# Kernel optimization log

Measured on AMD Instinct MI355X. Metric: run time of the kernel, lower is better.

Reference implementation:

```python
import jax, jax.numpy as jnp
import numpy as np

K = 3
C = 256
C4 = C // 4


def adaptive_avg_pool(x, k):
    # Faithful torch AdaptiveAvgPool2d: bin i covers [floor(i*H/k), ceil((i+1)*H/k))
    N, Ch, H, W = x.shape
    rows = []
    for i in range(k):
        sh, eh = (i * H) // k, -((-(i + 1) * H) // k)
        cols = []
        for j in range(k):
            sw, ew = (j * W) // k, -((-(j + 1) * W) // k)
            cols.append(x[:, :, sh:eh, sw:ew].mean(axis=(2, 3)))
        rows.append(jnp.stack(cols, axis=-1))  # [N,Ch,k]
    return jnp.stack(rows, axis=-2)  # [N,Ch,k,k]


def setup_inputs() -> dict:
    key = jax.random.key(0)
    ks = jax.random.split(key, 6)
    x = jax.random.normal(ks[0], (16, C, 128, 128), dtype=jnp.float32)
    # 1x1 convs stored as dense matrices (spatial 1x1 squeezed)
    conv_w = jax.random.normal(ks[1], (C4, C), dtype=jnp.float32) * (1.0 / np.sqrt(C))
    conv_b = jax.random.normal(ks[2], (C4,), dtype=jnp.float32) * 0.02
    dw_b = jax.random.normal(ks[3], (C4,), dtype=jnp.float32) * 0.02
    fuse_w = jax.random.normal(ks[4], (C, C4), dtype=jnp.float32) * (1.0 / np.sqrt(C4))
    fuse_b = jax.random.normal(ks[5], (C,), dtype=jnp.float32) * 0.02
    return {"x": x, "conv_w": conv_w, "conv_b": conv_b, "dw_b": dw_b,
            "fuse_w": fuse_w, "fuse_b": fuse_b}


def reference(x, conv_w, conv_b, dw_b, fuse_w, fuse_b):
    N, Ch, H, W = x.shape
    k = K
    c4 = conv_w.shape[0]
    # f = conv(x)  (1x1)
    f = jnp.einsum('nchw,oc->nohw', x, conv_w) + conv_b[None, :, None, None]
    # g = conv(pool(x)) -> per-sample depthwise filters [N, C4, k, k]
    xp = adaptive_avg_pool(x, k)
    g = jnp.einsum('nchw,oc->nohw', xp, conv_w) + conv_b[None, :, None, None]
    # batched dynamic depthwise conv: fold batch into groups, one fused conv
    p = (k - 1) // 2
    lhs = f.reshape(1, N * c4, H, W)
    rhs = g.reshape(N * c4, 1, k, k)
    y = jax.lax.conv_general_dilated(
        lhs, rhs, window_strides=(1, 1), padding=[(p, p), (p, p)],
        feature_group_count=N * c4,
        dimension_numbers=('NCHW', 'OIHW', 'NCHW'))
    y = y.reshape(N, c4, H, W) + dw_b[None, :, None, None]
    # fuse (1x1)
    out = jnp.einsum('nchw,oc->nohw', y, fuse_w) + fuse_b[None, :, None, None]
    return out
```

## Files before the change

kernel.cpp:

```cpp
#include <hip/hip_runtime.h>
#include <hip/hip_bf16.h>

#define NB 16
#define C 256
#define C4 64
#define HDIM 128
#define WDIM 128
#define HW 16384

typedef __bf16 bf16x8 __attribute__((ext_vector_type(8)));
typedef float f32x4 __attribute__((ext_vector_type(4)));

__device__ __forceinline__ unsigned short f2bf(float x) {
    union { __bf16 h; unsigned short u; } c;
    c.h = (__bf16)x;
    return c.u;
}
__device__ __forceinline__ float bf2f(unsigned short b) {
    union { float f; unsigned u; } a; a.u = ((unsigned)b) << 16; return a.f;
}

__global__ __launch_bounds__(256) void k0_pack(
    const float* __restrict__ conv_w, const float* __restrict__ fuse_w,
    const float* __restrict__ fuse_b, const float* __restrict__ dw_b,
    unsigned short* __restrict__ cwpk, unsigned short* __restrict__ fwpk,
    float* __restrict__ fbe)
{
    int tid = blockIdx.x * 256 + threadIdx.x;
    {
        int m = tid >> 8, k = tid & 255;
        int frag = (m >> 4) * 8 + (k >> 5);
        int lane = (m & 15) | (((k >> 3) & 3) << 4);
        int e = k & 7;
        cwpk[(frag * 64 + lane) * 8 + e] = f2bf(conv_w[m * 256 + k]);
    }
    {
        int m = tid >> 6, k = tid & 63;
        int frag = (m >> 4) * 2 + (k >> 5);
        int lane = (m & 15) | (((k >> 3) & 3) << 4);
        int e = k & 7;
        fwpk[(frag * 64 + lane) * 8 + e] = f2bf(fuse_w[m * 64 + k]);
    }
    if (tid < 256) {
        float s = fuse_b[tid];
        #pragma unroll
        for (int o = 0; o < 64; ++o) s += fuse_w[tid * 64 + o] * dw_b[o];
        fbe[tid] = s;
    }
}

__global__ __launch_bounds__(256) void k1_conv(
    const float* __restrict__ x, const unsigned short* __restrict__ cwpk,
    const float* __restrict__ conv_b, unsigned short* __restrict__ f_ws)
{
    __shared__ unsigned short xlds[32 * 138];
    int blk = blockIdx.x;
    int n = blk >> 7;
    int p0 = (blk & 127) * WDIM;
    int t = threadIdx.x;
    int lane = t & 63, wv = t >> 6, gq = lane >> 4, l15 = lane & 15;
    const float* xn = x + (size_t)n * C * HW + p0;

    int lch = t >> 5;
    int lpx = (t & 31) * 4;

    f32x4 r[4];
    #pragma unroll
    for (int j = 0; j < 4; ++j)
        r[j] = __builtin_nontemporal_load(
            reinterpret_cast<const f32x4*>(&xn[(size_t)(j * 8 + lch) * HW + lpx]));

    f32x4 acc[2][4];
    #pragma unroll
    for (int pt = 0; pt < 2; ++pt)
        #pragma unroll
        for (int m = 0; m < 4; ++m) acc[pt][m] = (f32x4){0.f, 0.f, 0.f, 0.f};

    for (int kc = 0; kc < 8; ++kc) {
        unsigned int pk[4][2];
        #pragma unroll
        for (int j = 0; j < 4; ++j) {
            pk[j][0] = ((unsigned)f2bf(r[j].y) << 16) | f2bf(r[j].x);
            pk[j][1] = ((unsigned)f2bf(r[j].w) << 16) | f2bf(r[j].z);
        }
        __syncthreads();
        #pragma unroll
        for (int j = 0; j < 4; ++j) {
            unsigned int* dst = reinterpret_cast<unsigned int*>(
                &xlds[(j * 8 + lch) * 138 + lpx]);
            dst[0] = pk[j][0];
            dst[1] = pk[j][1];
        }
        __syncthreads();
        if (kc < 7) {
            #pragma unroll
            for (int j = 0; j < 4; ++j)
                r[j] = __builtin_nontemporal_load(
                    reinterpret_cast<const f32x4*>(
                        &xn[(size_t)((kc + 1) * 32 + j * 8 + lch) * HW + lpx]));
        }
        bf16x8 a[4];
        #pragma unroll
        for (int m = 0; m < 4; ++m)
            a[m] = *reinterpret_cast<const bf16x8*>(cwpk + ((m * 8 + kc) * 64 + lane) * 8);
        #pragma unroll
        for (int pt = 0; pt < 2; ++pt) {
            int px = wv * 32 + pt * 16 + l15;
            union { bf16x8 v; unsigned short u[8]; } b;
            #pragma unroll
            for (int e = 0; e < 8; ++e)
                b.u[e] = xlds[(gq * 8 + e) * 138 + px];
            #pragma unroll
            for (int m = 0; m < 4; ++m)
                acc[pt][m] = __builtin_amdgcn_mfma_f32_16x16x32_bf16(a[m], b.v, acc[pt][m], 0, 0, 0);
        }
    }

    unsigned short* fn = f_ws + (size_t)n * C4 * HW;
    #pragma unroll
    for (int pt = 0; pt < 2; ++pt) {
        int px = p0 + wv * 32 + pt * 16 + l15;
        #pragma unroll
        for (int m = 0; m < 4; ++m) {
            #pragma unroll
            for (int e = 0; e < 4; ++e) {
                int o = m * 16 + gq * 4 + e;
                fn[(size_t)o * HW + px] = f2bf(acc[pt][m][e] + conv_b[o]);
            }
        }
    }
}

__global__ __launch_bounds__(256) void k2_pool(
    const unsigned short* __restrict__ f_ws, float* __restrict__ g_ws)
{
    int no = blockIdx.x;
    const unsigned short* fp = f_ws + (size_t)no * HW;
    int tid = threadIdx.x;
    float s[9];
    #pragma unroll
    for (int k = 0; k < 9; ++k) s[k] = 0.f;

    for (int it = 0; it < 8; ++it) {
        int p = (it * 256 + tid) * 8;
        int h = p >> 7, wbase = p & 127;
        union { uint4 q; unsigned short u[8]; } d;
        d.q = *reinterpret_cast<const uint4*>(fp + p);
        float cs0 = 0.f, cs1 = 0.f, cs2 = 0.f;
        #pragma unroll
        for (int z = 0; z < 8; ++z) {
            float v = bf2f(d.u[z]);
            int w = wbase + z;
            if (w < 43)            cs0 += v;
            if (w >= 42 && w < 86) cs1 += v;
            if (w >= 85)           cs2 += v;
        }
        if (h < 43)            { s[0] += cs0; s[1] += cs1; s[2] += cs2; }
        if (h >= 42 && h < 86) { s[3] += cs0; s[4] += cs1; s[5] += cs2; }
        if (h >= 85)           { s[6] += cs0; s[7] += cs1; s[8] += cs2; }
    }

    __shared__ float red[4][9];
    int lane = tid & 63, wv = tid >> 6;
    #pragma unroll
    for (int k = 0; k < 9; ++k) {
        float v = s[k];
        for (int off = 32; off > 0; off >>= 1) v += __shfl_down(v, off, 64);
        s[k] = v;
    }
    if (lane == 0) {
        #pragma unroll
        for (int k = 0; k < 9; ++k) red[wv][k] = s[k];
    }
    __syncthreads();
    if (tid < 9) {
        const int cnt[3] = {43, 44, 43};
        float tot = red[0][tid] + red[1][tid] + red[2][tid] + red[3][tid];
        int i = tid / 3, j = tid - 3 * i;
        g_ws[no * 9 + tid] = tot / (float)(cnt[i] * cnt[j]);
    }
}

__global__ __launch_bounds__(512) void k3_dwfuse(
    const unsigned short* __restrict__ f_ws, const float* __restrict__ g_ws,
    const unsigned short* __restrict__ fwpk, const float* __restrict__ fbe,
    float* __restrict__ out)
{
    __shared__ unsigned short ylds[64][136];
    int blk = blockIdx.x;
    int n = blk >> 7;
    int h = blk & 127;
    int t = threadIdx.x;

    {
        int o = t >> 3, q = t & 7;
        int wb = q * 16;
        const unsigned short* fp = f_ws + (size_t)(n * 64 + o) * HW;
        const float* gp = g_ws + (n * 64 + o) * 9;
        float gv[9];
        #pragma unroll
        for (int k = 0; k < 9; ++k) gv[k] = gp[k];
        float y[16];
        #pragma unroll
        for (int i = 0; i < 16; ++i) y[i] = 0.f;
        #pragma unroll
        for (int dy = -1; dy <= 1; ++dy) {
            int hh = h + dy;
            if (hh < 0 || hh >= HDIM) continue;
            const unsigned short* row = fp + hh * WDIM;
            union { uint4 q4; unsigned short u[8]; } bA, bB;
            bA.q4 = *reinterpret_cast<const uint4*>(row + wb);
            bB.q4 = *reinterpret_cast<const uint4*>(row + wb + 8);
            float lft = bf2f(row[wb == 0 ? 0 : wb - 1]);
            if (wb == 0)   lft = 0.f;
            float rgt = bf2f(row[wb == 112 ? 127 : wb + 16]);
            if (wb == 112) rgt = 0.f;
            float rv[18];
            rv[0] = lft;
            #pragma unroll
            for (int z = 0; z < 8; ++z) rv[1 + z] = bf2f(bA.u[z]);
            #pragma unroll
            for (int z = 0; z < 8; ++z) rv[9 + z] = bf2f(bB.u[z]);
            rv[17] = rgt;
            float g0 = gv[(dy + 1) * 3], g1 = gv[(dy + 1) * 3 + 1], g2 = gv[(dy + 1) * 3 + 2];
            #pragma unroll
            for (int i = 0; i < 16; ++i)
                y[i] += g0 * rv[i] + g1 * rv[i + 1] + g2 * rv[i + 2];
        }
        union { uint4 q4[2]; unsigned short u[16]; } pk;
        #pragma unroll
        for (int i = 0; i < 16; ++i) pk.u[i] = f2bf(y[i]);
        *reinterpret_cast<uint4*>(&ylds[o][wb])     = pk.q4[0];
        *reinterpret_cast<uint4*>(&ylds[o][wb + 8]) = pk.q4[1];
    }
    __syncthreads();

    int lane = t & 63, wv = t >> 6, gq = lane >> 4;
    int chb = (wv & 3) * 64, pxb = (wv >> 2) * 64;
    f32x4 acc[4][4];
    #pragma unroll
    for (int a = 0; a < 4; ++a)
        #pragma unroll
        for (int b = 0; b < 4; ++b) acc[a][b] = (f32x4){0.f,0.f,0.f,0.f};

    #pragma unroll
    for (int kc = 0; kc < 2; ++kc) {
        bf16x8 bfr[4];
        #pragma unroll
        for (int pj = 0; pj < 4; ++pj) {
            union { bf16x8 v; unsigned short u[8]; } bb;
            #pragma unroll
            for (int e = 0; e < 8; ++e)
                bb.u[e] = ylds[kc * 32 + gq * 8 + e][pxb + pj * 16 + (lane & 15)];
            bfr[pj] = bb.v;
        }
        #pragma unroll
        for (int mc = 0; mc < 4; ++mc) {
            int mtile = (wv & 3) * 4 + mc;
            bf16x8 a = *reinterpret_cast<const bf16x8*>(
                fwpk + ((mtile * 2 + kc) * 64 + lane) * 8);
            #pragma unroll
            for (int pj = 0; pj < 4; ++pj)
                acc[mc][pj] = __builtin_amdgcn_mfma_f32_16x16x32_bf16(a, bfr[pj], acc[mc][pj], 0, 0, 0);
        }
    }

    size_t outbase = (size_t)n * C * HW + (size_t)h * WDIM;
    #pragma unroll
    for (int mc = 0; mc < 4; ++mc) {
        #pragma unroll
        for (int e = 0; e < 4; ++e) {
            int c = chb + mc * 16 + gq * 4 + e;
            float bias = fbe[c];
            #pragma unroll
            for (int pj = 0; pj < 4; ++pj) {
                int w = pxb + pj * 16 + (lane & 15);
                out[outbase + (size_t)c * HW + w] = acc[mc][pj][e] + bias;
            }
        }
    }
}

extern "C" void kernel_launch(void* const* d_in, const int* in_sizes, int n_in,
                              void* d_out, int out_size, void* d_ws, size_t ws_size,
                              hipStream_t stream) {
    const float* x      = (const float*)d_in[0];
    const float* conv_w = (const float*)d_in[1];
    const float* conv_b = (const float*)d_in[2];
    const float* dw_b   = (const float*)d_in[3];
    const float* fuse_w = (const float*)d_in[4];
    const float* fuse_b = (const float*)d_in[5];
    float* out = (float*)d_out;

    char* ws = (char*)d_ws;
    unsigned short* f_ws = (unsigned short*)ws;
    float* g_ws          = (float*)(ws + 33554432);
    unsigned short* cwpk = (unsigned short*)(ws + 33554432 + 36864);
    unsigned short* fwpk = (unsigned short*)(ws + 33554432 + 36864 + 32768);
    float* fbe           = (float*)(ws + 33554432 + 36864 + 32768 + 32768);

    k0_pack<<<dim3(64), dim3(256), 0, stream>>>(conv_w, fuse_w, fuse_b, dw_b, cwpk, fwpk, fbe);
    k1_conv<<<dim3(2048), dim3(256), 0, stream>>>(x, cwpk, conv_b, f_ws);
    k2_pool<<<dim3(1024), dim3(256), 0, stream>>>(f_ws, g_ws);
    k3_dwfuse<<<dim3(2048), dim3(512), 0, stream>>>(f_ws, g_ws, fwpk, fbe, out);
}
```

Measured before the change: 140.8 us.

## Fuse adaptive pooling into conv kernel via atomics and vectorize stores

Removes the separate pooling kernel by accumulating per-row bin sums inside the 1x1 conv kernel and adding them into a zeroed global buffer with atomics; the depthwise kernel then scales by the bin counts. MFMA operands are swapped so each lane holds contiguous pixels, which allows packed 8-byte bf16 stores of f and 16-byte float4 stores of the output. This saves a full re-read of the f workspace and one launch, at the cost of atomic contention and float summation order that varies between runs.

```diff
diff --git a/kernel.cpp b/kernel.cpp
--- a/kernel.cpp
+++ b/kernel.cpp
@@ -24,7 +24,7 @@
     const float* __restrict__ conv_w, const float* __restrict__ fuse_w,
     const float* __restrict__ fuse_b, const float* __restrict__ dw_b,
     unsigned short* __restrict__ cwpk, unsigned short* __restrict__ fwpk,
-    float* __restrict__ fbe)
+    float* __restrict__ fbe, float* __restrict__ gsum)
 {
     int tid = blockIdx.x * 256 + threadIdx.x;
     {
@@ -47,16 +47,19 @@
         for (int o = 0; o < 64; ++o) s += fuse_w[tid * 64 + o] * dw_b[o];
         fbe[tid] = s;
     }
+    if (tid < NB * C4 * 9) gsum[tid] = 0.f;
 }
 
 __global__ __launch_bounds__(256) void k1_conv(
     const float* __restrict__ x, const unsigned short* __restrict__ cwpk,
-    const float* __restrict__ conv_b, unsigned short* __restrict__ f_ws)
+    const float* __restrict__ conv_b, unsigned short* __restrict__ f_ws,
+    float* __restrict__ gsum)
 {
     __shared__ unsigned short xlds[32 * 138];
     int blk = blockIdx.x;
     int n = blk >> 7;
-    int p0 = (blk & 127) * WDIM;
+    int h = blk & 127;
+    int p0 = h * WDIM;
     int t = threadIdx.x;
     int lane = t & 63, wv = t >> 6, gq = lane >> 4, l15 = lane & 15;
     const float* xn = x + (size_t)n * C * HW + p0;
@@ -112,77 +115,67 @@
                 b.u[e] = xlds[(gq * 8 + e) * 138 + px];
             #pragma unroll
             for (int m = 0; m < 4; ++m)
-                acc[pt][m] = __builtin_amdgcn_mfma_f32_16x16x32_bf16(a[m], b.v, acc[pt][m], 0, 0, 0);
-        }
-    }
+                acc[pt][m] = __builtin_amdgcn_mfma_f32_16x16x32_bf16(b.v, a[m], acc[pt][m], 0, 0, 0);
+        }
+    }
+
+    float cbv[4];
+    #pragma unroll
+    for (int m = 0; m < 4; ++m) cbv[m] = conv_b[m * 16 + l15];
+
+    float cs[4][3];
+    #pragma unroll
+    for (int m = 0; m < 4; ++m) cs[m][0] = cs[m][1] = cs[m][2] = 0.f;
 
     unsigned short* fn = f_ws + (size_t)n * C4 * HW;
     #pragma unroll
     for (int pt = 0; pt < 2; ++pt) {
-        int px = p0 + wv * 32 + pt * 16 + l15;
+        int pxb = wv * 32 + pt * 16 + gq * 4;
         #pragma unroll
         for (int m = 0; m < 4; ++m) {
+            int o = m * 16 + l15;
+            union { unsigned int d[2]; unsigned short u[4]; } pk2;
             #pragma unroll
             for (int e = 0; e < 4; ++e) {
-                int o = m * 16 + gq * 4 + e;
-                fn[(size_t)o * HW + px] = f2bf(acc[pt][m][e] + conv_b[o]);
+                float v = acc[pt][m][e] + cbv[m];
+                pk2.u[e] = f2bf(v);
+                int px = pxb + e;
+                if (px < 43)              cs[m][0] += v;
+                if (px >= 42 && px < 86)  cs[m][1] += v;
+                if (px >= 85)             cs[m][2] += v;
             }
-        }
-    }
-}
-
-__global__ __launch_bounds__(256) void k2_pool(
-    const unsigned short* __restrict__ f_ws, float* __restrict__ g_ws)
-{
-    int no = blockIdx.x;
-    const unsigned short* fp = f_ws + (size_t)no * HW;
-    int tid = threadIdx.x;
-    float s[9];
-    #pragma unroll
-    for (int k = 0; k < 9; ++k) s[k] = 0.f;
-
-    for (int it = 0; it < 8; ++it) {
-        int p = (it * 256 + tid) * 8;
-        int h = p >> 7, wbase = p & 127;
-        union { uint4 q; unsigned short u[8]; } d;
-        d.q = *reinterpret_cast<const uint4*>(fp + p);
-        float cs0 = 0.f, cs1 = 0.f, cs2 = 0.f;
-        #pragma unroll
-        for (int z = 0; z < 8; ++z) {
-            float v = bf2f(d.u[z]);
-            int w = wbase + z;
-            if (w < 43)            cs0 += v;
-            if (w >= 42 && w < 86) cs1 += v;
-            if (w >= 85)           cs2 += v;
-        }
-        if (h < 43)            { s[0] += cs0; s[1] += cs1; s[2] += cs2; }
-        if (h >= 42 && h < 86) { s[3] += cs0; s[4] += cs1; s[5] += cs2; }
-        if (h >= 85)           { s[6] += cs0; s[7] += cs1; s[8] += cs2; }
-    }
-
-    __shared__ float red[4][9];
-    int lane = tid & 63, wv = tid >> 6;
-    #pragma unroll
-    for (int k = 0; k < 9; ++k) {
-        float v = s[k];
-        for (int off = 32; off > 0; off >>= 1) v += __shfl_down(v, off, 64);
-        s[k] = v;
-    }
-    if (lane == 0) {
-        #pragma unroll
-        for (int k = 0; k < 9; ++k) red[wv][k] = s[k];
-    }
-    __syncthreads();
-    if (tid < 9) {
-        const int cnt[3] = {43, 44, 43};
-        float tot = red[0][tid] + red[1][tid] + red[2][tid] + red[3][tid];
-        int i = tid / 3, j = tid - 3 * i;
-        g_ws[no * 9 + tid] = tot / (float)(cnt[i] * cnt[j]);
+            *reinterpret_cast<uint2*>(&fn[(size_t)o * HW + p0 + pxb]) =
+                (uint2){pk2.d[0], pk2.d[1]};
+        }
+    }
+
+    #pragma unroll
+    for (int m = 0; m < 4; ++m)
+        #pragma unroll
+        for (int b = 0; b < 3; ++b) {
+            float v = cs[m][b];
+            v += __shfl_xor(v, 16, 64);
+            v += __shfl_xor(v, 32, 64);
+            cs[m][b] = v;
+        }
+
+    if (gq == 0) {
+        int hbA = (h < 43) ? 0 : (h < 86 ? 1 : 2);
+        int hbB = (h == 42) ? 1 : ((h == 85) ? 2 : -1);
+        #pragma unroll
+        for (int m = 0; m < 4; ++m) {
+            int base = (n * 64 + m * 16 + l15) * 9;
+            #pragma unroll
+            for (int b = 0; b < 3; ++b) {
+                atomicAdd(&gsum[base + hbA * 3 + b], cs[m][b]);
+                if (hbB >= 0) atomicAdd(&gsum[base + hbB * 3 + b], cs[m][b]);
+            }
+        }
     }
 }
 
 __global__ __launch_bounds__(512) void k3_dwfuse(
-    const unsigned short* __restrict__ f_ws, const float* __restrict__ g_ws,
+    const unsigned short* __restrict__ f_ws, const float* __restrict__ gsum,
     const unsigned short* __restrict__ fwpk, const float* __restrict__ fbe,
     float* __restrict__ out)
 {
@@ -193,13 +186,17 @@
     int t = threadIdx.x;
 
     {
+        const float ginv[9] = {
+            1.f/1849.f, 1.f/1892.f, 1.f/1849.f,
+            1.f/1892.f, 1.f/1936.f, 1.f/1892.f,
+            1.f/1849.f, 1.f/1892.f, 1.f/1849.f };
         int o = t >> 3, q = t & 7;
         int wb = q * 16;
         const unsigned short* fp = f_ws + (size_t)(n * 64 + o) * HW;
-        const float* gp = g_ws + (n * 64 + o) * 9;
+        const float* gp = gsum + (n * 64 + o) * 9;
         float gv[9];
         #pragma unroll
-        for (int k = 0; k < 9; ++k) gv[k] = gp[k];
+        for (int k = 0; k < 9; ++k) gv[k] = gp[k] * ginv[k];
         float y[16];
         #pragma unroll
         for (int i = 0; i < 16; ++i) y[i] = 0.f;
@@ -235,7 +232,7 @@
     }
     __syncthreads();
 
-    int lane = t & 63, wv = t >> 6, gq = lane >> 4;
+    int lane = t & 63, wv = t >> 6, gq = lane >> 4, l15 = lane & 15;
     int chb = (wv & 3) * 64, pxb = (wv >> 2) * 64;
     f32x4 acc[4][4];
     #pragma unroll
@@ -251,7 +248,7 @@
             union { bf16x8 v; unsigned short u[8]; } bb;
             #pragma unroll
             for (int e = 0; e < 8; ++e)
-                bb.u[e] = ylds[kc * 32 + gq * 8 + e][pxb + pj * 16 + (lane & 15)];
+                bb.u[e] = ylds[kc * 32 + gq * 8 + e][pxb + pj * 16 + l15];
             bfr[pj] = bb.v;
         }
         #pragma unroll
@@ -261,22 +258,22 @@
                 fwpk + ((mtile * 2 + kc) * 64 + lane) * 8);
             #pragma unroll
             for (int pj = 0; pj < 4; ++pj)
-                acc[mc][pj] = __builtin_amdgcn_mfma_f32_16x16x32_bf16(a, bfr[pj], acc[mc][pj], 0, 0, 0);
+                acc[mc][pj] = __builtin_amdgcn_mfma_f32_16x16x32_bf16(bfr[pj], a, acc[mc][pj], 0, 0, 0);
         }
     }
 
     size_t outbase = (size_t)n * C * HW + (size_t)h * WDIM;
     #pragma unroll
     for (int mc = 0; mc < 4; ++mc) {
-        #pragma unroll
-        for (int e = 0; e < 4; ++e) {
-            int c = chb + mc * 16 + gq * 4 + e;
-            float bias = fbe[c];
-            #pragma unroll
-            for (int pj = 0; pj < 4; ++pj) {
-                int w = pxb + pj * 16 + (lane & 15);
-                out[outbase + (size_t)c * HW + w] = acc[mc][pj][e] + bias;
-            }
+        int c = chb + mc * 16 + l15;
+        float bias = fbe[c];
+        #pragma unroll
+        for (int pj = 0; pj < 4; ++pj) {
+            int w = pxb + pj * 16 + gq * 4;
+            f32x4 vv;
+            #pragma unroll
+            for (int e = 0; e < 4; ++e) vv[e] = acc[mc][pj][e] + bias;
+            *reinterpret_cast<f32x4*>(&out[outbase + (size_t)c * HW + w]) = vv;
         }
     }
 }
@@ -294,13 +291,12 @@
 
     char* ws = (char*)d_ws;
     unsigned short* f_ws = (unsigned short*)ws;
-    float* g_ws          = (float*)(ws + 33554432);
+    float* gsum          = (float*)(ws + 33554432);
     unsigned short* cwpk = (unsigned short*)(ws + 33554432 + 36864);
     unsigned short* fwpk = (unsigned short*)(ws + 33554432 + 36864 + 32768);
     float* fbe           = (float*)(ws + 33554432 + 36864 + 32768 + 32768);
 
-    k0_pack<<<dim3(64), dim3(256), 0, stream>>>(conv_w, fuse_w, fuse_b, dw_b, cwpk, fwpk, fbe);
-    k1_conv<<<dim3(2048), dim3(256), 0, stream>>>(x, cwpk, conv_b, f_ws);
-    k2_pool<<<dim3(1024), dim3(256), 0, stream>>>(f_ws, g_ws);
-    k3_dwfuse<<<dim3(2048), dim3(512), 0, stream>>>(f_ws, g_ws, fwpk, fbe, out);
-}
+    k0_pack<<<dim3(64), dim3(256), 0, stream>>>(conv_w, fuse_w, fuse_b, dw_b, cwpk, fwpk, fbe, gsum);
+    k1_conv<<<dim3(2048), dim3(256), 0, stream>>>(x, cwpk, conv_b, f_ws, gsum);
+    k3_dwfuse<<<dim3(2048), dim3(512), 0, stream>>>(f_ws, gsum, fwpk, fbe, out);
+}
```

New measurement: 260.8 us. 85.3% more time.
